# Optimization experiments

Hardware: AMD Instinct MI355X
Metric: run time of the kernel (lower is better)

Reference implementation:

```python
import jax, jax.numpy as jnp
import numpy as np

NUM_HEADS = 16
HEAD_DIM = 64
PATCH_NUMS = [1, 2, 3, 4, 5, 6, 8, 10, 13, 16, 32]
MAX_SCALE_MUL = float(np.log(100.0))


def precompute_freqs_cis(dim, patch_nums, theta=10000.0):
    # Returns [L, dim//2, 2] (cos, sin) pairs; matches torch.polar construction.
    freqs = 1.0 / theta ** (np.arange(0, dim, 4)[: dim // 4].astype(np.float32) / dim)  # [dim//4]
    tx, ty = [], []
    grid = 32.0
    for p in patch_nums:
        ix, iy = np.meshgrid(np.arange(p), np.arange(p), indexing="ij")  # torch default 'ij'
        tx.append(ix.flatten().astype(np.float32) / p * grid)
        ty.append(iy.flatten().astype(np.float32) / p * grid)
    tx = np.concatenate(tx)
    ty = np.concatenate(ty)
    ang = np.concatenate([np.outer(tx, freqs), np.outer(ty, freqs)], axis=1).astype(np.float32)  # [L, dim//2]
    return np.stack([np.cos(ang), np.sin(ang)], axis=-1)  # [L, dim//2, 2]


FREQS_CIS_CROSS = jnp.asarray(precompute_freqs_cis(HEAD_DIM, [12]))  # [144, 32, 2]


def _rope(x, cis):
    # x: [B, H, S, D]; cis: [S, D//2, 2] -> complex multiply on (even, odd) pairs.
    B, H, S, D = x.shape
    xr = x.reshape(B, H, S, D // 2, 2)
    a, b = xr[..., 0], xr[..., 1]
    c = cis[..., 0][None, None]  # [1,1,S,D//2]
    d = cis[..., 1][None, None]
    return jnp.stack([a * c - b * d, a * d + b * c], axis=-1).reshape(B, H, S, D)


def setup_inputs() -> dict:
    key = jax.random.key(0)
    ks = jax.random.split(key, 6)
    B, C, Ck, Lk = 8, 1024, 1024, 144
    fc = precompute_freqs_cis(HEAD_DIM, PATCH_NUMS)
    L = fc.shape[0]  # 1704
    return {
        "x": jax.random.normal(ks[0], (B, L, C), jnp.float32),
        "y": jax.random.normal(ks[1], (B, Lk, Ck), jnp.float32),
        "freqs_cis": jnp.asarray(fc),
        "attn_bias": jax.random.normal(ks[2], (1, 1, L, Lk), jnp.float32) * 0.1,
        "Wq": jax.random.normal(ks[3], (C, C), jnp.float32) * 0.02,
        "q_bias": jnp.zeros((C,), jnp.float32),
        "Wkv": jax.random.normal(ks[4], (2 * C, Ck), jnp.float32) * 0.02,
        "v_bias": jnp.zeros((C,), jnp.float32),
        "Wproj": jax.random.normal(ks[5], (C, C), jnp.float32) * 0.02,
        "b_proj": jnp.zeros((C,), jnp.float32),
        "scale_mul": jnp.full((1, NUM_HEADS, 1, 1), np.log(4.0), jnp.float32),
    }


def reference(x, y, freqs_cis, attn_bias, Wq, q_bias, Wkv, v_bias, Wproj, b_proj, scale_mul):
    B, L, C = x.shape
    H, D = NUM_HEADS, HEAD_DIM
    Lk = y.shape[1]
    # fused QKV projections (k bias is the zero buffer)
    q = (x @ Wq.T + q_bias).reshape(B, L, H, D).transpose(0, 2, 1, 3)  # [B,H,L,D]
    kv_bias = jnp.concatenate([jnp.zeros_like(v_bias), v_bias])
    kv = (y @ Wkv.T + kv_bias).reshape(B, Lk, 2, H, D)
    k = kv[:, :, 0].transpose(0, 2, 1, 3)  # [B,H,Lk,D]
    v = kv[:, :, 1].transpose(0, 2, 1, 3)
    # attn_l2_norm path: scale = 1, per-head learned multiplier
    sm = jnp.exp(jnp.minimum(scale_mul, MAX_SCALE_MUL))  # [1,H,1,1]
    q = q / jnp.maximum(jnp.linalg.norm(q, axis=-1, keepdims=True), 1e-12) * sm
    k = k / jnp.maximum(jnp.linalg.norm(k, axis=-1, keepdims=True), 1e-12)
    # inline RoPE (cross freqs recomputed from 12x12 grid every forward in the original)
    q = _rope(q, freqs_cis)
    k = _rope(k, FREQS_CIS_CROSS)
    # manual (non-flash) masked attention, scale = 1 due to l2 norm
    logits = jnp.einsum("bhld,bhkd->bhlk", q, k) + attn_bias
    attn = jax.nn.softmax(logits, axis=-1)
    oup = jnp.einsum("bhlk,bhkd->bhld", attn, v).transpose(0, 2, 1, 3).reshape(B, L, C)
    return oup @ Wproj.T + b_proj
```

## Files before the change

### kernel.cpp

```cpp
#include <hip/hip_runtime.h>

using u16 = unsigned short;
using u32 = unsigned int;

typedef __bf16 bf16x8 __attribute__((ext_vector_type(8)));
typedef float  f32x4  __attribute__((ext_vector_type(4)));
typedef _Float16 f16;
typedef _Float16 f16x4 __attribute__((ext_vector_type(4)));
typedef _Float16 f16x8 __attribute__((ext_vector_type(8)));
typedef u16 u16x4 __attribute__((ext_vector_type(4)));

__device__ __forceinline__ float b2f(u16 u) { return __uint_as_float(((u32)u) << 16); }
__device__ __forceinline__ u16 f2b(float f) {
    u32 u = __float_as_uint(f);
    return (u16)((u + 0x7FFFu + ((u >> 16) & 1u)) >> 16);
}

__device__ __forceinline__ void async_cp16(void* lds, const void* g) {
    __builtin_amdgcn_global_load_lds(
        (const __attribute__((address_space(1))) u32*)g,
        (__attribute__((address_space(3))) u32*)lds, 16, 0, 0);
}

__global__ __launch_bounds__(256) void split_f32(const float* __restrict__ src,
                                                 u16* __restrict__ hi,
                                                 u16* __restrict__ lo, int n4) {
    int i = blockIdx.x * 256 + threadIdx.x;
    if (i >= n4) return;
    f32x4 v = reinterpret_cast<const f32x4*>(src)[i];
    u16x4 H, L;
#pragma unroll
    for (int j = 0; j < 4; j++) {
        u16 hb = f2b(v[j]);
        H[j] = hb;
        L[j] = f2b(v[j] - b2f(hb));
    }
    reinterpret_cast<u16x4*>(hi)[i] = H;
    reinterpret_cast<u16x4*>(lo)[i] = L;
}

__global__ __launch_bounds__(256) void cvt_f16(const float* __restrict__ src,
                                               f16* __restrict__ dst, int n4) {
    int i = blockIdx.x * 256 + threadIdx.x;
    if (i >= n4) return;
    f32x4 v = reinterpret_cast<const f32x4*>(src)[i];
    f16x4 h = {(f16)v[0], (f16)v[1], (f16)v[2], (f16)v[3]};
    reinterpret_cast<f16x4*>(dst)[i] = h;
}

__device__ __forceinline__ void split8(f32x4 a0, f32x4 a1, bf16x8& hi, bf16x8& lo) {
    union { bf16x8 v; u16 s[8]; } H, L;
#pragma unroll
    for (int j = 0; j < 4; j++) {
        float f = a0[j]; u16 hb = f2b(f); H.s[j] = hb;     L.s[j] = f2b(f - b2f(hb));
        float g = a1[j]; u16 gb = f2b(g); H.s[4 + j] = gb; L.s[4 + j] = f2b(g - b2f(gb));
    }
    hi = H.v; lo = L.v;
}

__global__ __launch_bounds__(512) void gemm_q(const u16* __restrict__ xhi,
                                              const u16* __restrict__ xlo,
                                              const u16* __restrict__ whi,
                                              const u16* __restrict__ wlo,
                                              const float* __restrict__ qb,
                                              const float* __restrict__ fc,
                                              const float* __restrict__ smul,
                                              f16* __restrict__ qout) {
    const int K = 1024, L = 1704;
    __shared__ u16 xs[2][2][64][64];
    int tid = threadIdx.x;
    int lane = tid & 63, wv = tid >> 6;
    int mt = blockIdx.x >> 1;
    int hg = blockIdx.x & 1;
    int h  = hg * 8 + wv;
    int lr = lane & 15, quad = lane >> 4;
    long m0 = (long)mt * 64;

    int srow = tid >> 3, scol = (tid & 7) * 8;
    const u16* g_hi = xhi + (m0 + srow) * K + scol;
    const u16* g_lo = xlo + (m0 + srow) * K + scol;
    u16* l_hi0 = &xs[0][0][srow][scol];
    u16* l_lo0 = &xs[0][1][srow][scol];
    u16* l_hi1 = &xs[1][0][srow][scol];
    u16* l_lo1 = &xs[1][1][srow][scol];

    const bf16x8* wh_p[4];
    const bf16x8* wl_p[4];
#pragma unroll
    for (int i = 0; i < 4; i++) {
        long woff = ((long)(h * 64 + i * 16 + lr)) * K;
        wh_p[i] = reinterpret_cast<const bf16x8*>(whi + woff) + quad;
        wl_p[i] = reinterpret_cast<const bf16x8*>(wlo + woff) + quad;
    }

    f32x4 acc[4][4] = {};

    async_cp16(l_hi0, g_hi);
    async_cp16(l_lo0, g_lo);
    __syncthreads();

    for (int c = 0; c < 16; c++) {
        if (c < 15) {
            const u16* gh = g_hi + (c + 1) * 64;
            const u16* gl = g_lo + (c + 1) * 64;
            if (c & 1) { async_cp16(l_hi0, gh); async_cp16(l_lo0, gl); }
            else       { async_cp16(l_hi1, gh); async_cp16(l_lo1, gl); }
        }
        int buf = c & 1;
#pragma unroll
        for (int s = 0; s < 2; s++) {
            bf16x8 AH[4], AL[4], WH[4], WL[4];
#pragma unroll
            for (int i = 0; i < 4; i++) {
                WH[i] = wh_p[i][c * 8 + s * 4];
                WL[i] = wl_p[i][c * 8 + s * 4];
            }
#pragma unroll
            for (int i = 0; i < 4; i++) {
                AH[i] = *reinterpret_cast<const bf16x8*>(&xs[buf][0][i * 16 + lr][s * 32 + quad * 8]);
                AL[i] = *reinterpret_cast<const bf16x8*>(&xs[buf][1][i * 16 + lr][s * 32 + quad * 8]);
            }
#pragma unroll
            for (int mi = 0; mi < 4; mi++)
#pragma unroll
                for (int ni = 0; ni < 4; ni++) {
                    acc[mi][ni] = __builtin_amdgcn_mfma_f32_16x16x32_bf16(AH[mi], WH[ni], acc[mi][ni], 0, 0, 0);
                    acc[mi][ni] = __builtin_amdgcn_mfma_f32_16x16x32_bf16(AL[mi], WH[ni], acc[mi][ni], 0, 0, 0);
                    acc[mi][ni] = __builtin_amdgcn_mfma_f32_16x16x32_bf16(AH[mi], WL[ni], acc[mi][ni], 0, 0, 0);
                }
        }
        __syncthreads();
    }

    float sm = __expf(fminf(smul[h], 4.6051702f));
#pragma unroll
    for (int mi = 0; mi < 4; mi++) {
#pragma unroll
        for (int r = 0; r < 4; r++) {
            long rowg = m0 + mi * 16 + quad * 4 + r;
            float v[4];
            float ss = 0.f;
#pragma unroll
            for (int ni = 0; ni < 4; ni++) {
                v[ni] = acc[mi][ni][r] + qb[h * 64 + ni * 16 + lr];
                ss += v[ni] * v[ni];
            }
            ss += __shfl_xor(ss, 1, 64); ss += __shfl_xor(ss, 2, 64);
            ss += __shfl_xor(ss, 4, 64); ss += __shfl_xor(ss, 8, 64);
            float inv = sm / fmaxf(sqrtf(ss), 1e-12f);
            int l = (int)(rowg % L);
            f16* orow = qout + rowg * 1024 + h * 64;
#pragma unroll
            for (int ni = 0; ni < 4; ni++) {
                float u = v[ni] * inv;
                int d = ni * 16 + lr;
                int j = d >> 1;
                float c = fc[(l * 32 + j) * 2];
                float s = fc[(l * 32 + j) * 2 + 1];
                float pr = __shfl_xor(u, 1, 64);
                float o = (lane & 1) ? (pr * s + u * c) : (u * c - pr * s);
                orow[d] = (f16)o;
            }
        }
    }
}

__constant__ double FREQS16[16] = {
    1.0, 0.5623413251903491, 0.31622776601683794, 0.17782794100389228,
    0.1, 0.05623413251903491, 0.03162277660168379, 0.017782794100389228,
    0.01, 0.005623413251903491, 0.0031622776601683794, 0.0017782794100389228,
    0.001, 0.0005623413251903491, 0.00031622776601683794, 0.00017782794100389228};

__global__ __launch_bounds__(256) void gemm_kv(const float* __restrict__ y,
                                               const float* __restrict__ Wkv,
                                               const float* __restrict__ vb,
                                               f16* __restrict__ khp,
                                               f16* __restrict__ klp,
                                               f16* __restrict__ vhp,
                                               f16* __restrict__ vlp) {
    const int K = 1024;
    int lane = threadIdx.x & 63, wv = threadIdx.x >> 6;
    int mt = blockIdx.x >> 3;
    int nt = (blockIdx.x & 7) * 4 + wv;
    int lr = lane & 15, quad = lane >> 4;
    long m0 = (long)mt * 64;

    const float* arow[4];
    const float* wrow[4];
#pragma unroll
    for (int i = 0; i < 4; i++) {
        arow[i] = y   + (m0 + i * 16 + lr) * K + quad * 8;
        wrow[i] = Wkv + ((long)(nt * 64 + i * 16 + lr)) * K + quad * 8;
    }

    f32x4 acc[4][4] = {};
    for (int ks = 0; ks < 32; ks++) {
        bf16x8 ah[4], al[4], wh[4], wl[4];
#pragma unroll
        for (int i = 0; i < 4; i++) {
            const float* ap = arow[i] + ks * 32;
            split8(*(const f32x4*)ap, *(const f32x4*)(ap + 4), ah[i], al[i]);
            const float* wp = wrow[i] + ks * 32;
            split8(*(const f32x4*)wp, *(const f32x4*)(wp + 4), wh[i], wl[i]);
        }
#pragma unroll
        for (int mi = 0; mi < 4; mi++)
#pragma unroll
            for (int ni = 0; ni < 4; ni++) {
                acc[mi][ni] = __builtin_amdgcn_mfma_f32_16x16x32_bf16(ah[mi], wh[ni], acc[mi][ni], 0, 0, 0);
                acc[mi][ni] = __builtin_amdgcn_mfma_f32_16x16x32_bf16(al[mi], wh[ni], acc[mi][ni], 0, 0, 0);
                acc[mi][ni] = __builtin_amdgcn_mfma_f32_16x16x32_bf16(ah[mi], wl[ni], acc[mi][ni], 0, 0, 0);
            }
    }

    bool isv = nt >= 16;
    int h = isv ? nt - 16 : nt;
#pragma unroll
    for (int mi = 0; mi < 4; mi++) {
#pragma unroll
        for (int r = 0; r < 4; r++) {
            long row = m0 + mi * 16 + quad * 4 + r;
            int b = (int)(row / 144), lk = (int)(row % 144);
            long bh = b * 16 + h;
            float v[4];
#pragma unroll
            for (int ni = 0; ni < 4; ni++)
                v[ni] = acc[mi][ni][r] + (isv ? vb[h * 64 + ni * 16 + lr] : 0.f);
            if (!isv) {
                float ss = v[0] * v[0] + v[1] * v[1] + v[2] * v[2] + v[3] * v[3];
                ss += __shfl_xor(ss, 1, 64); ss += __shfl_xor(ss, 2, 64);
                ss += __shfl_xor(ss, 4, 64); ss += __shfl_xor(ss, 8, 64);
                float inv = 1.f / fmaxf(sqrtf(ss), 1e-12f);
                f16* kh_row = khp + (bh * 144 + lk) * 64;
                f16* kl_row = klp + (bh * 144 + lk) * 64;
#pragma unroll
                for (int ni = 0; ni < 4; ni++) {
                    float u = v[ni] * inv;
                    int d = ni * 16 + lr;
                    int j = d >> 1;
                    int f = j & 15;
                    float tc = (j < 16) ? ((float)(lk / 12)) / 12.0f * 32.0f
                                        : ((float)(lk % 12)) / 12.0f * 32.0f;
                    float ang = (float)((double)tc * FREQS16[f]);
                    float c = cosf(ang), s = sinf(ang);
                    float pr = __shfl_xor(u, 1, 64);
                    float o = (lane & 1) ? (pr * s + u * c) : (u * c - pr * s);
                    f16 oh = (f16)o;
                    f16 ol = (f16)(o - (float)oh);
                    kh_row[d] = oh;
                    kl_row[d] = ol;
                }
            } else {
#pragma unroll
                for (int ni = 0; ni < 4; ni++) {
                    float val = v[ni];
                    int d = ni * 16 + lr;
                    f16 vh = (f16)val;
                    f16 vl = (f16)(val - (float)vh);
                    vhp[(bh * 64 + d) * 144 + lk] = vh;
                    vlp[(bh * 64 + d) * 144 + lk] = vl;
                }
            }
        }
    }
}

__global__ __launch_bounds__(256, 3) void attn(const f16* q,
                                               const f16* __restrict__ khp,
                                               const f16* __restrict__ klp,
                                               const f16* __restrict__ vhp,
                                               const f16* __restrict__ vlp,
                                               const float* __restrict__ abias,
                                               f16* aout) {
    const int L = 1704;
    __shared__ __align__(16) f16 ps[4][16][152];
    int tid = threadIdx.x;
    int lane = tid & 63, wv = tid >> 6;
    int lr = lane & 15, quad = lane >> 4;
    int ltile = blockIdx.x % 27;
    int bh = blockIdx.x / 27;
    int h = bh & 15, b = bh >> 4;
    int l0 = ltile * 64;
    int rows = min(64, L - l0);

    int rA = wv * 16 + lr;
    int rAc = min(rA, rows - 1);
    const f16* qrow = q + ((long)(b * L + l0 + rAc)) * 1024 + h * 64;
    f16x8 qa0 = *reinterpret_cast<const f16x8*>(qrow + quad * 8);
    f16x8 qa1 = *reinterpret_cast<const f16x8*>(qrow + 32 + quad * 8);

    const f16* khb = khp + (long)bh * (144 * 64);
    const f16* klb = klp + (long)bh * (144 * 64);

    f32x4 acc[9] = {};
#pragma unroll
    for (int t = 0; t < 9; t++) {
        const f16* k0 = khb + (t * 16 + lr) * 64 + quad * 8;
        const f16* k1 = klb + (t * 16 + lr) * 64 + quad * 8;
        f16x8 bh0 = *reinterpret_cast<const f16x8*>(k0);
        f16x8 bh1 = *reinterpret_cast<const f16x8*>(k0 + 32);
        f16x8 bl0 = *reinterpret_cast<const f16x8*>(k1);
        f16x8 bl1 = *reinterpret_cast<const f16x8*>(k1 + 32);
        acc[t] = __builtin_amdgcn_mfma_f32_16x16x32_f16(qa0, bh0, acc[t], 0, 0, 0);
        acc[t] = __builtin_amdgcn_mfma_f32_16x16x32_f16(qa1, bh1, acc[t], 0, 0, 0);
        acc[t] = __builtin_amdgcn_mfma_f32_16x16x32_f16(qa0, bl0, acc[t], 0, 0, 0);
        acc[t] = __builtin_amdgcn_mfma_f32_16x16x32_f16(qa1, bl1, acc[t], 0, 0, 0);
    }

    int rC = wv * 16 + quad * 4;
#pragma unroll
    for (int r = 0; r < 4; r++) {
        long lrow = (long)(l0 + min(rC + r, rows - 1)) * 144;
#pragma unroll
        for (int t = 0; t < 9; t++) acc[t][r] += abias[lrow + t * 16 + lr];
    }

#pragma unroll
    for (int r = 0; r < 4; r++) {
        float mx = acc[0][r];
#pragma unroll
        for (int t = 1; t < 9; t++) mx = fmaxf(mx, acc[t][r]);
        mx = fmaxf(mx, __shfl_xor(mx, 1, 64));
        mx = fmaxf(mx, __shfl_xor(mx, 2, 64));
        mx = fmaxf(mx, __shfl_xor(mx, 4, 64));
        mx = fmaxf(mx, __shfl_xor(mx, 8, 64));
        float s = 0.f;
#pragma unroll
        for (int t = 0; t < 9; t++) {
            float e = __expf(acc[t][r] - mx);
            acc[t][r] = e;
            s += e;
        }
        s += __shfl_xor(s, 1, 64);
        s += __shfl_xor(s, 2, 64);
        s += __shfl_xor(s, 4, 64);
        s += __shfl_xor(s, 8, 64);
        float inv = 1.0f / s;
#pragma unroll
        for (int t = 0; t < 9; t++)
            ps[wv][quad * 4 + r][t * 16 + lr] = (f16)(acc[t][r] * inv);
    }

    const f16* vhb = vhp + (long)bh * (64 * 144);
    const f16* vlb = vlp + (long)bh * (64 * 144);
    f32x4 oacc[4] = {};
#pragma unroll
    for (int ks = 0; ks < 5; ks++) {
        f16x8 pa = {0, 0, 0, 0, 0, 0, 0, 0};
        if (ks < 4 || quad < 2)
            pa = *reinterpret_cast<const f16x8*>(&ps[wv][lr][ks * 32 + quad * 8]);
#pragma unroll
        for (int n = 0; n < 4; n++) {
            f16x8 vh8 = {0, 0, 0, 0, 0, 0, 0, 0};
            f16x8 vl8 = {0, 0, 0, 0, 0, 0, 0, 0};
            if (ks < 4 || quad < 2) {
                const f16* vr  = vhb + (n * 16 + lr) * 144 + ks * 32 + quad * 8;
                const f16* vr2 = vlb + (n * 16 + lr) * 144 + ks * 32 + quad * 8;
                vh8 = *reinterpret_cast<const f16x8*>(vr);
                vl8 = *reinterpret_cast<const f16x8*>(vr2);
            }
            oacc[n] = __builtin_amdgcn_mfma_f32_16x16x32_f16(pa, vh8, oacc[n], 0, 0, 0);
            oacc[n] = __builtin_amdgcn_mfma_f32_16x16x32_f16(pa, vl8, oacc[n], 0, 0, 0);
        }
    }

    long ob = (long)(b * L + l0);
#pragma unroll
    for (int r = 0; r < 4; r++) {
        int rw = rC + r;
        if (rw < rows) {
            f16* ao = aout + (ob + rw) * 1024 + h * 64;
#pragma unroll
            for (int n = 0; n < 4; n++) ao[n * 16 + lr] = (f16)oacc[n][r];
        }
    }
}

__global__ __launch_bounds__(512) void gemm_proj(const f16* __restrict__ A,
                                                 const f16* __restrict__ Wh,
                                                 const float* __restrict__ bias,
                                                 float* __restrict__ out) {
    const int K = 1024;
    __shared__ f16 as[2][64][64];
    int tid = threadIdx.x;
    int lane = tid & 63, wv = tid >> 6;
    int mt = blockIdx.x >> 1;
    int cg = blockIdx.x & 1;
    int lr = lane & 15, quad = lane >> 4;
    long m0 = (long)mt * 64;
    long n0 = (long)cg * 512 + wv * 64;

    int srow = tid >> 3, scol = (tid & 7) * 8;
    const f16* g_a = A + (m0 + srow) * K + scol;
    f16* l_a0 = &as[0][srow][scol];
    f16* l_a1 = &as[1][srow][scol];

    const f16x8* wrow[4];
#pragma unroll
    for (int i = 0; i < 4; i++)
        wrow[i] = reinterpret_cast<const f16x8*>(Wh + (n0 + i * 16 + lr) * K) + quad;

    f32x4 acc[4][4] = {};

    async_cp16(l_a0, g_a);
    __syncthreads();

    for (int c = 0; c < 16; c++) {
        if (c < 15) {
            const f16* ga = g_a + (c + 1) * 64;
            if (c & 1) async_cp16(l_a0, ga);
            else       async_cp16(l_a1, ga);
        }
        int buf = c & 1;
#pragma unroll
        for (int s = 0; s < 2; s++) {
            f16x8 af[4], wf[4];
#pragma unroll
            for (int i = 0; i < 4; i++) wf[i] = wrow[i][c * 8 + s * 4];
#pragma unroll
            for (int i = 0; i < 4; i++)
                af[i] = *reinterpret_cast<const f16x8*>(&as[buf][i * 16 + lr][s * 32 + quad * 8]);
#pragma unroll
            for (int mi = 0; mi < 4; mi++)
#pragma unroll
                for (int ni = 0; ni < 4; ni++)
                    acc[mi][ni] = __builtin_amdgcn_mfma_f32_16x16x32_f16(af[mi], wf[ni], acc[mi][ni], 0, 0, 0);
        }
        __syncthreads();
    }

#pragma unroll
    for (int ni = 0; ni < 4; ni++) {
        int col = (int)n0 + ni * 16 + lr;
        float b = bias[col];
#pragma unroll
        for (int mi = 0; mi < 4; mi++) {
            long row = m0 + mi * 16 + quad * 4;
#pragma unroll
            for (int r = 0; r < 4; r++)
                out[(row + r) * 1024 + col] = acc[mi][ni][r] + b;
        }
    }
}

extern "C" void kernel_launch(void* const* d_in, const int* in_sizes, int n_in,
                              void* d_out, int out_size, void* d_ws, size_t ws_size,
                              hipStream_t stream) {
    const float* x     = (const float*)d_in[0];
    const float* y     = (const float*)d_in[1];
    const float* fc    = (const float*)d_in[2];
    const float* abias = (const float*)d_in[3];
    const float* Wq    = (const float*)d_in[4];
    const float* qb    = (const float*)d_in[5];
    const float* Wkv   = (const float*)d_in[6];
    const float* vb    = (const float*)d_in[7];
    const float* Wp    = (const float*)d_in[8];
    const float* bp    = (const float*)d_in[9];
    const float* smul  = (const float*)d_in[10];

    const long XN = 13959168L;
    const long WN = 1048576L;
    const long KVN = 1179648L;

    f16* qbuf  = (f16*)d_ws;
    u16* wq_hi = (u16*)(qbuf + XN);
    u16* wq_lo = wq_hi + WN;
    f16* wp_h  = (f16*)(wq_lo + WN);

    u16* x_hi = (u16*)d_out;
    u16* x_lo = x_hi + XN;
    f16* kh_p  = (f16*)d_out;
    f16* kl_p  = kh_p + KVN;
    f16* vth_p = kl_p + KVN;
    f16* vtl_p = vth_p + KVN;

    dim3 blk(256);
    split_f32<<<dim3((int)(XN / 4 / 256)), blk, 0, stream>>>(x, x_hi, x_lo, (int)(XN / 4));
    split_f32<<<dim3((int)(WN / 4 / 256)), blk, 0, stream>>>(Wq, wq_hi, wq_lo, (int)(WN / 4));
    cvt_f16  <<<dim3((int)(WN / 4 / 256)), blk, 0, stream>>>(Wp, wp_h, (int)(WN / 4));
    gemm_q<<<dim3(426), dim3(512), 0, stream>>>(x_hi, x_lo, wq_hi, wq_lo, qb, fc, smul, qbuf);
    gemm_kv<<<dim3(144), blk, 0, stream>>>(y, Wkv, vb, kh_p, kl_p, vth_p, vtl_p);
    attn<<<dim3(3456), blk, 0, stream>>>(qbuf, kh_p, kl_p, vth_p, vtl_p, abias, (f16*)qbuf);
    gemm_proj<<<dim3(426), dim3(512), 0, stream>>>((const f16*)qbuf, wp_h, bp, (float*)d_out);
}
```

Baseline: 598.2 us.

## Fuse prep conversions, swizzle LDS tiles, and halve GEMM block size

The three fp32 split/convert launches are merged into a single prep kernel. gemm_q and gemm_proj now run 256-thread blocks covering 4 heads or 256 columns each, so twice as many blocks are launched. Both GEMMs also XOR-swizzle the LDS tile layout so that the A-fragment reads avoid bank conflicts. The goals are lower launch overhead, fewer LDS conflicts and better occupancy and load balance. The cost is that the x tile is now loaded from global memory twice as many times across blocks.

```diff
diff --git a/kernel.cpp b/kernel.cpp
--- a/kernel.cpp
+++ b/kernel.cpp
@@ -22,11 +22,7 @@
         (__attribute__((address_space(3))) u32*)lds, 16, 0, 0);
 }
 
-__global__ __launch_bounds__(256) void split_f32(const float* __restrict__ src,
-                                                 u16* __restrict__ hi,
-                                                 u16* __restrict__ lo, int n4) {
-    int i = blockIdx.x * 256 + threadIdx.x;
-    if (i >= n4) return;
+__device__ __forceinline__ void split4_store(const float* src, u16* hi, u16* lo, int i) {
     f32x4 v = reinterpret_cast<const f32x4*>(src)[i];
     u16x4 H, L;
 #pragma unroll
@@ -39,13 +35,26 @@
     reinterpret_cast<u16x4*>(lo)[i] = L;
 }
 
-__global__ __launch_bounds__(256) void cvt_f16(const float* __restrict__ src,
-                                               f16* __restrict__ dst, int n4) {
+__global__ __launch_bounds__(256) void prep(const float* __restrict__ x,
+                                            const float* __restrict__ Wq,
+                                            const float* __restrict__ Wp,
+                                            u16* __restrict__ xhi, u16* __restrict__ xlo,
+                                            u16* __restrict__ wqhi, u16* __restrict__ wqlo,
+                                            f16* __restrict__ wph,
+                                            int nx4, int nw4) {
     int i = blockIdx.x * 256 + threadIdx.x;
-    if (i >= n4) return;
-    f32x4 v = reinterpret_cast<const f32x4*>(src)[i];
-    f16x4 h = {(f16)v[0], (f16)v[1], (f16)v[2], (f16)v[3]};
-    reinterpret_cast<f16x4*>(dst)[i] = h;
+    if (i < nx4) {
+        split4_store(x, xhi, xlo, i);
+    } else if (i < nx4 + nw4) {
+        split4_store(Wq, wqhi, wqlo, i - nx4);
+    } else {
+        int k = i - nx4 - nw4;
+        if (k < nw4) {
+            f32x4 v = reinterpret_cast<const f32x4*>(Wp)[k];
+            f16x4 h = {(f16)v[0], (f16)v[1], (f16)v[2], (f16)v[3]};
+            reinterpret_cast<f16x4*>(wph)[k] = h;
+        }
+    }
 }
 
 __device__ __forceinline__ void split8(f32x4 a0, f32x4 a1, bf16x8& hi, bf16x8& lo) {
@@ -58,7 +67,7 @@
     hi = H.v; lo = L.v;
 }
 
-__global__ __launch_bounds__(512) void gemm_q(const u16* __restrict__ xhi,
+__global__ __launch_bounds__(256) void gemm_q(const u16* __restrict__ xhi,
                                               const u16* __restrict__ xlo,
                                               const u16* __restrict__ whi,
                                               const u16* __restrict__ wlo,
@@ -70,19 +79,24 @@
     __shared__ u16 xs[2][2][64][64];
     int tid = threadIdx.x;
     int lane = tid & 63, wv = tid >> 6;
-    int mt = blockIdx.x >> 1;
-    int hg = blockIdx.x & 1;
-    int h  = hg * 8 + wv;
+    int mt = blockIdx.x >> 2;
+    int hg = blockIdx.x & 3;
+    int h  = hg * 4 + wv;
     int lr = lane & 15, quad = lane >> 4;
     long m0 = (long)mt * 64;
 
-    int srow = tid >> 3, scol = (tid & 7) * 8;
-    const u16* g_hi = xhi + (m0 + srow) * K + scol;
-    const u16* g_lo = xlo + (m0 + srow) * K + scol;
-    u16* l_hi0 = &xs[0][0][srow][scol];
-    u16* l_lo0 = &xs[0][1][srow][scol];
-    u16* l_hi1 = &xs[1][0][srow][scol];
-    u16* l_lo1 = &xs[1][1][srow][scol];
+    int r0 = tid >> 3, c0 = tid & 7;
+    int s1 = tid + 256;
+    int r1 = s1 >> 3, c1 = s1 & 7;
+    const u16* srch0 = xhi + (m0 + r0) * K + ((c0 ^ (r0 & 7)) * 8);
+    const u16* srch1 = xhi + (m0 + r1) * K + ((c1 ^ (r1 & 7)) * 8);
+    const u16* srcl0 = xlo + (m0 + r0) * K + ((c0 ^ (r0 & 7)) * 8);
+    const u16* srcl1 = xlo + (m0 + r1) * K + ((c1 ^ (r1 & 7)) * 8);
+    u16* dh[2][2]; u16* dl[2][2];
+    dh[0][0] = &xs[0][0][r0][c0 * 8]; dh[0][1] = &xs[0][0][r1][c1 * 8];
+    dh[1][0] = &xs[1][0][r0][c0 * 8]; dh[1][1] = &xs[1][0][r1][c1 * 8];
+    dl[0][0] = &xs[0][1][r0][c0 * 8]; dl[0][1] = &xs[0][1][r1][c1 * 8];
+    dl[1][0] = &xs[1][1][r0][c0 * 8]; dl[1][1] = &xs[1][1][r1][c1 * 8];
 
     const bf16x8* wh_p[4];
     const bf16x8* wl_p[4];
@@ -93,22 +107,26 @@
         wl_p[i] = reinterpret_cast<const bf16x8*>(wlo + woff) + quad;
     }
 
+    int sp0 = ((0 + quad) ^ (lr & 7)) * 8;
+    int sp1 = ((4 + quad) ^ (lr & 7)) * 8;
+
     f32x4 acc[4][4] = {};
 
-    async_cp16(l_hi0, g_hi);
-    async_cp16(l_lo0, g_lo);
+    async_cp16(dh[0][0], srch0); async_cp16(dh[0][1], srch1);
+    async_cp16(dl[0][0], srcl0); async_cp16(dl[0][1], srcl1);
     __syncthreads();
 
     for (int c = 0; c < 16; c++) {
         if (c < 15) {
-            const u16* gh = g_hi + (c + 1) * 64;
-            const u16* gl = g_lo + (c + 1) * 64;
-            if (c & 1) { async_cp16(l_hi0, gh); async_cp16(l_lo0, gl); }
-            else       { async_cp16(l_hi1, gh); async_cp16(l_lo1, gl); }
+            int nb = (c + 1) & 1;
+            int off = (c + 1) * 64;
+            async_cp16(dh[nb][0], srch0 + off); async_cp16(dh[nb][1], srch1 + off);
+            async_cp16(dl[nb][0], srcl0 + off); async_cp16(dl[nb][1], srcl1 + off);
         }
         int buf = c & 1;
 #pragma unroll
         for (int s = 0; s < 2; s++) {
+            int sp = s ? sp1 : sp0;
             bf16x8 AH[4], AL[4], WH[4], WL[4];
 #pragma unroll
             for (int i = 0; i < 4; i++) {
@@ -117,8 +135,8 @@
             }
 #pragma unroll
             for (int i = 0; i < 4; i++) {
-                AH[i] = *reinterpret_cast<const bf16x8*>(&xs[buf][0][i * 16 + lr][s * 32 + quad * 8]);
-                AL[i] = *reinterpret_cast<const bf16x8*>(&xs[buf][1][i * 16 + lr][s * 32 + quad * 8]);
+                AH[i] = *reinterpret_cast<const bf16x8*>(&xs[buf][0][i * 16 + lr][sp]);
+                AL[i] = *reinterpret_cast<const bf16x8*>(&xs[buf][1][i * 16 + lr][sp]);
             }
 #pragma unroll
             for (int mi = 0; mi < 4; mi++)
@@ -376,7 +394,7 @@
     }
 }
 
-__global__ __launch_bounds__(512) void gemm_proj(const f16* __restrict__ A,
+__global__ __launch_bounds__(256) void gemm_proj(const f16* __restrict__ A,
                                                  const f16* __restrict__ Wh,
                                                  const float* __restrict__ bias,
                                                  float* __restrict__ out) {
@@ -384,42 +402,52 @@
     __shared__ f16 as[2][64][64];
     int tid = threadIdx.x;
     int lane = tid & 63, wv = tid >> 6;
-    int mt = blockIdx.x >> 1;
-    int cg = blockIdx.x & 1;
+    int mt = blockIdx.x >> 2;
+    int cg = blockIdx.x & 3;
     int lr = lane & 15, quad = lane >> 4;
     long m0 = (long)mt * 64;
-    long n0 = (long)cg * 512 + wv * 64;
-
-    int srow = tid >> 3, scol = (tid & 7) * 8;
-    const f16* g_a = A + (m0 + srow) * K + scol;
-    f16* l_a0 = &as[0][srow][scol];
-    f16* l_a1 = &as[1][srow][scol];
+    long n0 = (long)cg * 256 + wv * 64;
+
+    int r0 = tid >> 3, c0 = tid & 7;
+    int s1i = tid + 256;
+    int r1 = s1i >> 3, c1 = s1i & 7;
+    const f16* srca0 = A + (m0 + r0) * K + ((c0 ^ (r0 & 7)) * 8);
+    const f16* srca1 = A + (m0 + r1) * K + ((c1 ^ (r1 & 7)) * 8);
+    f16* da[2][2];
+    da[0][0] = &as[0][r0][c0 * 8]; da[0][1] = &as[0][r1][c1 * 8];
+    da[1][0] = &as[1][r0][c0 * 8]; da[1][1] = &as[1][r1][c1 * 8];
 
     const f16x8* wrow[4];
 #pragma unroll
     for (int i = 0; i < 4; i++)
         wrow[i] = reinterpret_cast<const f16x8*>(Wh + (n0 + i * 16 + lr) * K) + quad;
 
+    int sp0 = ((0 + quad) ^ (lr & 7)) * 8;
+    int sp1 = ((4 + quad) ^ (lr & 7)) * 8;
+
     f32x4 acc[4][4] = {};
 
-    async_cp16(l_a0, g_a);
+    async_cp16(da[0][0], srca0);
+    async_cp16(da[0][1], srca1);
     __syncthreads();
 
     for (int c = 0; c < 16; c++) {
         if (c < 15) {
-            const f16* ga = g_a + (c + 1) * 64;
-            if (c & 1) async_cp16(l_a0, ga);
-            else       async_cp16(l_a1, ga);
+            int nb = (c + 1) & 1;
+            int off = (c + 1) * 64;
+            async_cp16(da[nb][0], srca0 + off);
+            async_cp16(da[nb][1], srca1 + off);
         }
         int buf = c & 1;
 #pragma unroll
         for (int s = 0; s < 2; s++) {
+            int sp = s ? sp1 : sp0;
             f16x8 af[4], wf[4];
 #pragma unroll
             for (int i = 0; i < 4; i++) wf[i] = wrow[i][c * 8 + s * 4];
 #pragma unroll
             for (int i = 0; i < 4; i++)
-                af[i] = *reinterpret_cast<const f16x8*>(&as[buf][i * 16 + lr][s * 32 + quad * 8]);
+                af[i] = *reinterpret_cast<const f16x8*>(&as[buf][i * 16 + lr][sp]);
 #pragma unroll
             for (int mi = 0; mi < 4; mi++)
 #pragma unroll
@@ -474,12 +502,14 @@
     f16* vth_p = kl_p + KVN;
     f16* vtl_p = vth_p + KVN;
 
-    dim3 blk(256);
-    split_f32<<<dim3((int)(XN / 4 / 256)), blk, 0, stream>>>(x, x_hi, x_lo, (int)(XN / 4));
-    split_f32<<<dim3((int)(WN / 4 / 256)), blk, 0, stream>>>(Wq, wq_hi, wq_lo, (int)(WN / 4));
-    cvt_f16  <<<dim3((int)(WN / 4 / 256)), blk, 0, stream>>>(Wp, wp_h, (int)(WN / 4));
-    gemm_q<<<dim3(426), dim3(512), 0, stream>>>(x_hi, x_lo, wq_hi, wq_lo, qb, fc, smul, qbuf);
-    gemm_kv<<<dim3(144), blk, 0, stream>>>(y, Wkv, vb, kh_p, kl_p, vth_p, vtl_p);
-    attn<<<dim3(3456), blk, 0, stream>>>(qbuf, kh_p, kl_p, vth_p, vtl_p, abias, (f16*)qbuf);
-    gemm_proj<<<dim3(426), dim3(512), 0, stream>>>((const f16*)qbuf, wp_h, bp, (float*)d_out);
-}
+    int nx4 = (int)(XN / 4);
+    int nw4 = (int)(WN / 4);
+    int prep_blocks = (nx4 + 2 * nw4) / 256;
+
+    prep<<<dim3(prep_blocks), dim3(256), 0, stream>>>(x, Wq, Wp, x_hi, x_lo,
+                                                      wq_hi, wq_lo, wp_h, nx4, nw4);
+    gemm_q<<<dim3(852), dim3(256), 0, stream>>>(x_hi, x_lo, wq_hi, wq_lo, qb, fc, smul, qbuf);
+    gemm_kv<<<dim3(144), dim3(256), 0, stream>>>(y, Wkv, vb, kh_p, kl_p, vth_p, vtl_p);
+    attn<<<dim3(3456), dim3(256), 0, stream>>>(qbuf, kh_p, kl_p, vth_p, vtl_p, abias, (f16*)qbuf);
+    gemm_proj<<<dim3(852), dim3(256), 0, stream>>>((const f16*)qbuf, wp_h, bp, (float*)d_out);
+}
```

Measured after the change: 586.2 us. 1.02x faster.
